# Kernel tuning notes

Measured on AMD Instinct MI355X. Metric: run time of the kernel, lower is better.

## Reference

```python
import jax, jax.numpy as jnp
import numpy as np

B, S, H, HEADS = 2, 512, 768, 12
HD = H // HEADS  # head dim 64
LN_EPS = 1e-5


def setup_inputs() -> dict:
    key = jax.random.key(0)
    ks = jax.random.split(key, 8)
    w = lambda k, shape: jax.random.normal(k, shape, dtype=jnp.float32) * 0.02
    return {
        "hidden_states": jax.random.normal(ks[0], (B, S, H), dtype=jnp.float32),
        "attention_mask": jnp.ones((B, S), dtype=jnp.int32),
        "Wp": w(ks[1], (H, H)), "bp": jnp.zeros((H,), jnp.float32),   # input_projection
        "Wq": w(ks[2], (H, H)), "bq": jnp.zeros((H,), jnp.float32),   # MHA q in-proj
        "Wk": w(ks[3], (H, H)), "bk": jnp.zeros((H,), jnp.float32),   # MHA k in-proj
        "We": w(ks[4], (H, H)), "be": jnp.zeros((H,), jnp.float32),   # edge_projection
        "gamma": jnp.ones((H,), jnp.float32), "beta": jnp.zeros((H,), jnp.float32),
    }


def reference(hidden_states, attention_mask, Wp, bp, Wq, bq, Wk, bk, We, be, gamma, beta):
    b, s, _ = hidden_states.shape
    # input projection (dropout = identity at eval)
    node = hidden_states @ Wp.T + bp                                   # [B,S,H]

    # self-attention weights (per-head), key_padding_mask = ~attention_mask
    q = (node @ Wq.T + bq).reshape(b, s, HEADS, HD).transpose(0, 2, 1, 3)
    k = (node @ Wk.T + bk).reshape(b, s, HEADS, HD).transpose(0, 2, 1, 3)
    logits = jnp.einsum("bhqd,bhkd->bhqk", q, k) / jnp.sqrt(jnp.float32(HD))
    pad = (attention_mask == 0)                                        # [B,S] keys to mask
    logits = jnp.where(pad[:, None, None, :], jnp.float32(-1e9), logits)
    attn = jax.nn.softmax(logits, axis=-1)                             # [B,HEADS,S,S]
    avg = attn.mean(axis=1)                                            # [B,S,S]

    # top-k sparsification: k = S // 2 neighbors per node
    ktop = s // 2
    _, idx = jax.lax.top_k(avg, ktop)                                  # [B,S,ktop]
    idx = jnp.sort(idx, axis=-1)  # torch.where emits dst in ascending order per src row
    scores = jnp.take_along_axis(avg, idx, axis=-1)                    # [B,S,ktop]

    # edge index with per-batch node offsets (all-ones mask -> every row kept)
    src = jnp.broadcast_to(jnp.arange(s)[None, :, None], (b, s, ktop))
    offset = (jnp.arange(b) * s)[:, None, None]
    edge_index = jnp.stack([(src + offset).reshape(-1),
                            (idx + offset).reshape(-1)], axis=0)       # [2, B*S*ktop]

    # edge_attr: zeros with col 0 = attn score, then Linear  ==  score * We[:,0] + be
    edge_attr = scores.reshape(-1)[:, None] * We[:, 0][None, :] + be   # [E, H]

    # final layer norm on node features
    mu = node.mean(axis=-1, keepdims=True)
    var = ((node - mu) ** 2).mean(axis=-1, keepdims=True)
    node_features = (node - mu) * jax.lax.rsqrt(var + LN_EPS) * gamma + beta

    return node_features, edge_index, edge_attr
```

## Files before the change

### kernel.cpp

```cpp
#include <hip/hip_runtime.h>

#define HH 768
#define SS 512
#define NB 2
#define NHEADS 12
#define KTOP 256
#define ETOT (NB*SS*KTOP)
#define LN_EPS 1e-5f

#define EI_OFF 786432L
#define EA_OFF 1310720L
#define PSZ    786432L

#define FMA16(a,b) \
    acc[0][0]=fmaf(a.x,b.x,acc[0][0]); acc[0][1]=fmaf(a.x,b.y,acc[0][1]); \
    acc[0][2]=fmaf(a.x,b.z,acc[0][2]); acc[0][3]=fmaf(a.x,b.w,acc[0][3]); \
    acc[1][0]=fmaf(a.y,b.x,acc[1][0]); acc[1][1]=fmaf(a.y,b.y,acc[1][1]); \
    acc[1][2]=fmaf(a.y,b.z,acc[1][2]); acc[1][3]=fmaf(a.y,b.w,acc[1][3]); \
    acc[2][0]=fmaf(a.z,b.x,acc[2][0]); acc[2][1]=fmaf(a.z,b.y,acc[2][1]); \
    acc[2][2]=fmaf(a.z,b.z,acc[2][2]); acc[2][3]=fmaf(a.z,b.w,acc[2][3]); \
    acc[3][0]=fmaf(a.w,b.x,acc[3][0]); acc[3][1]=fmaf(a.w,b.y,acc[3][1]); \
    acc[3][2]=fmaf(a.w,b.z,acc[3][2]); acc[3][3]=fmaf(a.w,b.w,acc[3][3]);

#define STORE_TILE(DST, V0, V1) \
    (DST)[sc4*4+0][srow]    = (V0).x; (DST)[sc4*4+1][srow]    = (V0).y; \
    (DST)[sc4*4+2][srow]    = (V0).z; (DST)[sc4*4+3][srow]    = (V0).w; \
    (DST)[sc4*4+0][srow+32] = (V1).x; (DST)[sc4*4+1][srow+32] = (V1).y; \
    (DST)[sc4*4+2][srow+32] = (V1).z; (DST)[sc4*4+3][srow+32] = (V1).w;

__device__ __forceinline__ float4 f4sum(const float* __restrict__ p0,
                                        const float* __restrict__ p1,
                                        const float* __restrict__ b,
                                        long off, int bcol)
{
    const float4 x = *(const float4*)(p0 + off);
    const float4 y = *(const float4*)(p1 + off);
    const float4 z = *(const float4*)(b + bcol);
    float4 r;
    r.x = x.x + y.x + z.x; r.y = x.y + y.y + z.y;
    r.z = x.z + y.z + z.z; r.w = x.w + y.w + z.w;
    return r;
}

__global__ __launch_bounds__(256, 3) void gemm_sk1(
    const float* __restrict__ A, const float* __restrict__ W,
    float* __restrict__ P)
{
    __shared__ float As[2][32][68];
    __shared__ float Ws[2][32][68];
    const int tid = threadIdx.x;
    const int tm = tid >> 4, tn = tid & 15;
    const int m0 = blockIdx.y * 64, n0 = blockIdx.x * 64;
    const int kh = blockIdx.z;
    const int srow = tid >> 3, sc4 = tid & 7;
    const int kbeg = kh * 384;

    const float* Ar0 = A + (long)(m0 + srow) * HH + kbeg + sc4 * 4;
    const float* Ar1 = Ar0 + 32 * HH;
    const float* Wr0 = W + (long)(n0 + srow) * HH + kbeg + sc4 * 4;
    const float* Wr1 = Wr0 + 32 * HH;

    float4 pa0 = *(const float4*)Ar0, pa1 = *(const float4*)Ar1;
    float4 pw0 = *(const float4*)Wr0, pw1 = *(const float4*)Wr1;

    float acc[4][4] = {};
    for (int kt = 0; kt < 12; ++kt) {
        const int cur = kt & 1;
        STORE_TILE(As[cur], pa0, pa1);
        STORE_TILE(Ws[cur], pw0, pw1);
        __syncthreads();
        if (kt < 11) {
            const int off = (kt + 1) * 32;
            pa0 = *(const float4*)(Ar0 + off);
            pa1 = *(const float4*)(Ar1 + off);
            pw0 = *(const float4*)(Wr0 + off);
            pw1 = *(const float4*)(Wr1 + off);
        }
        #pragma unroll
        for (int k = 0; k < 32; ++k) {
            const float4 a = *(const float4*)&As[cur][k][tm*4];
            const float4 b = *(const float4*)&Ws[cur][k][tn*4];
            FMA16(a, b)
        }
    }

    float* C = P + (long)kh * PSZ + (long)m0 * HH + n0;
    #pragma unroll
    for (int i = 0; i < 4; ++i) {
        float4 r;
        r.x = acc[i][0]; r.y = acc[i][1]; r.z = acc[i][2]; r.w = acc[i][3];
        *(float4*)(C + (long)(tm*4 + i) * HH + tn * 4) = r;
    }
}

__global__ __launch_bounds__(256, 3) void gemm_sk2(
    const float* __restrict__ P, const float* __restrict__ bp,
    const float* __restrict__ Wq, const float* __restrict__ Wk,
    float* __restrict__ QKP)
{
    __shared__ float As[2][32][68];
    __shared__ float Ws[2][32][68];
    const int tid = threadIdx.x;
    const int tm = tid >> 4, tn = tid & 15;
    const int m0 = blockIdx.y * 64, n0 = blockIdx.x * 64;
    const int sel = blockIdx.z >> 1, kh = blockIdx.z & 1;
    const float* W = sel ? Wk : Wq;
    const int srow = tid >> 3, sc4 = tid & 7;
    const int kbeg = kh * 384;

    const float* P1 = P + PSZ;
    const long aoff0 = (long)(m0 + srow) * HH + kbeg + sc4 * 4;
    const long aoff1 = aoff0 + 32 * HH;
    const int  bcol  = kbeg + sc4 * 4;
    const float* Wr0 = W + (long)(n0 + srow) * HH + kbeg + sc4 * 4;
    const float* Wr1 = Wr0 + 32 * HH;

    float4 pa0 = f4sum(P, P1, bp, aoff0, bcol);
    float4 pa1 = f4sum(P, P1, bp, aoff1, bcol);
    float4 pw0 = *(const float4*)Wr0;
    float4 pw1 = *(const float4*)Wr1;

    float acc[4][4] = {};
    for (int kt = 0; kt < 12; ++kt) {
        const int cur = kt & 1;
        STORE_TILE(As[cur], pa0, pa1);
        STORE_TILE(Ws[cur], pw0, pw1);
        __syncthreads();
        if (kt < 11) {
            const int off = (kt + 1) * 32;
            pa0 = f4sum(P, P1, bp, aoff0 + off, bcol + off);
            pa1 = f4sum(P, P1, bp, aoff1 + off, bcol + off);
            pw0 = *(const float4*)(Wr0 + off);
            pw1 = *(const float4*)(Wr1 + off);
        }
        #pragma unroll
        for (int k = 0; k < 32; ++k) {
            const float4 a = *(const float4*)&As[cur][k][tm*4];
            const float4 b = *(const float4*)&Ws[cur][k][tn*4];
            FMA16(a, b)
        }
    }

    float* C = QKP + ((long)sel * 2 + kh) * PSZ + (long)m0 * HH + n0;
    #pragma unroll
    for (int i = 0; i < 4; ++i) {
        float4 r;
        r.x = acc[i][0]; r.y = acc[i][1]; r.z = acc[i][2]; r.w = acc[i][3];
        *(float4*)(C + (long)(tm*4 + i) * HH + tn * 4) = r;
    }
}

__global__ __launch_bounds__(256, 3) void gemm_qk2(
    const float* __restrict__ QKP, const float* __restrict__ bq,
    const float* __restrict__ bk, float* __restrict__ logits)
{
    __shared__ float As[2][32][68];
    __shared__ float Ws[2][32][68];
    const int tid = threadIdx.x;
    const int tm = tid >> 4, tn = tid & 15;
    const int m0 = blockIdx.y * 64, n0 = blockIdx.x * 64;
    const int z = blockIdx.z, bz = z / NHEADS, hz = z - bz * NHEADS;
    const int srow = tid >> 3, sc4 = tid & 7;

    const float* q0 = QKP;
    const float* q1 = QKP + PSZ;
    const float* k0 = QKP + 2 * PSZ;
    const float* k1 = QKP + 3 * PSZ;

    const long rbase = (long)bz * SS * HH + hz * 64;
    const long aoff0 = rbase + (long)(m0 + srow) * HH + sc4 * 4;
    const long aoff1 = aoff0 + 32 * HH;
    const long woff0 = rbase + (long)(n0 + srow) * HH + sc4 * 4;
    const long woff1 = woff0 + 32 * HH;
    const int  bcol  = hz * 64 + sc4 * 4;

    float4 pa0 = f4sum(q0, q1, bq, aoff0, bcol);
    float4 pa1 = f4sum(q0, q1, bq, aoff1, bcol);
    float4 pw0 = f4sum(k0, k1, bk, woff0, bcol);
    float4 pw1 = f4sum(k0, k1, bk, woff1, bcol);

    float acc[4][4] = {};
    for (int kt = 0; kt < 2; ++kt) {
        const int cur = kt & 1;
        STORE_TILE(As[cur], pa0, pa1);
        STORE_TILE(Ws[cur], pw0, pw1);
        __syncthreads();
        if (kt == 0) {
            pa0 = f4sum(q0, q1, bq, aoff0 + 32, bcol + 32);
            pa1 = f4sum(q0, q1, bq, aoff1 + 32, bcol + 32);
            pw0 = f4sum(k0, k1, bk, woff0 + 32, bcol + 32);
            pw1 = f4sum(k0, k1, bk, woff1 + 32, bcol + 32);
        }
        #pragma unroll
        for (int k = 0; k < 32; ++k) {
            const float4 a = *(const float4*)&As[cur][k][tm*4];
            const float4 b = *(const float4*)&Ws[cur][k][tn*4];
            FMA16(a, b)
        }
    }

    float* C = logits + (long)z * SS * SS;
    #pragma unroll
    for (int i = 0; i < 4; ++i) {
        float4 r;
        r.x = acc[i][0] * 0.125f;
        r.y = acc[i][1] * 0.125f;
        r.z = acc[i][2] * 0.125f;
        r.w = acc[i][3] * 0.125f;
        *(float4*)(C + (long)(m0 + tm*4 + i) * SS + n0 + tn * 4) = r;
    }
}

__global__ __launch_bounds__(256) void ln_sum(
    const float* __restrict__ P, const float* __restrict__ bp,
    const float* __restrict__ gamma, const float* __restrict__ beta,
    float* __restrict__ out)
{
    const int row = blockIdx.x;
    const int t   = threadIdx.x;
    const float* x0 = P + (long)row * HH;
    const float* x1 = x0 + PSZ;

    const float v0 = x0[t]       + x1[t]       + bp[t];
    const float v1 = x0[t + 256] + x1[t + 256] + bp[t + 256];
    const float v2 = x0[t + 512] + x1[t + 512] + bp[t + 512];
    float s  = v0 + v1 + v2;
    float sq = v0 * v0 + v1 * v1 + v2 * v2;

    __shared__ float rs_[4], rq_[4];
    #pragma unroll
    for (int o = 32; o >= 1; o >>= 1) {
        s  += __shfl_xor(s, o);
        sq += __shfl_xor(sq, o);
    }
    if ((t & 63) == 0) { rs_[t >> 6] = s; rq_[t >> 6] = sq; }
    __syncthreads();
    const float S = rs_[0] + rs_[1] + rs_[2] + rs_[3];
    const float Q = rq_[0] + rq_[1] + rq_[2] + rq_[3];
    const float mu  = S * (1.f / HH);
    const float var = Q * (1.f / HH) - mu * mu;
    const float inv = rsqrtf(var + LN_EPS);

    float* o = out + (long)row * HH;
    o[t]       = (v0 - mu) * inv * gamma[t]       + beta[t];
    o[t + 256] = (v1 - mu) * inv * gamma[t + 256] + beta[t + 256];
    o[t + 512] = (v2 - mu) * inv * gamma[t + 512] + beta[t + 512];
}

__global__ __launch_bounds__(256) void attn_edge(
    const float* __restrict__ logits,
    const int*   __restrict__ mask,
    const float* __restrict__ We, const float* __restrict__ be,
    float* __restrict__ ei,
    float* __restrict__ ea)
{
    const int row = blockIdx.x;
    const int b   = row >> 9;
    const int qi  = row & 511;
    const int t   = threadIdx.x;
    const int wid = t >> 6, lane = t & 63;

    __shared__ float redA[4], redB[4];
    __shared__ unsigned long long keys[SS];
    __shared__ float4 wt[192], bt[192];
    __shared__ unsigned long long mskS[8];
    __shared__ float ssel[KTOP];

    const bool m0 = mask[b * SS + t] != 0;
    const bool m1 = mask[b * SS + t + 256] != 0;

    const float* basep = logits + ((long)b * NHEADS * SS + qi) * SS;

    float a0 = 0.f, a1 = 0.f;
    float c0v = m0 ? basep[t]       : -1e9f;
    float c1v = m1 ? basep[t + 256] : -1e9f;
    for (int h = 0; h < NHEADS; ++h) {
        const float l0 = c0v, l1 = c1v;
        if (h + 1 < NHEADS) {
            const float* nr = basep + (long)(h + 1) * SS * SS;
            c0v = m0 ? nr[t]       : -1e9f;
            c1v = m1 ? nr[t + 256] : -1e9f;
        }
        float v = fmaxf(l0, l1);
        #pragma unroll
        for (int o = 32; o >= 1; o >>= 1) v = fmaxf(v, __shfl_xor(v, o));
        if (lane == 0) redA[wid] = v;
        __syncthreads();
        const float bm = fmaxf(fmaxf(redA[0], redA[1]), fmaxf(redA[2], redA[3]));
        const float x0 = __expf(l0 - bm);
        const float x1 = __expf(l1 - bm);
        float s = x0 + x1;
        #pragma unroll
        for (int o = 32; o >= 1; o >>= 1) s += __shfl_xor(s, o);
        if (lane == 0) redB[wid] = s;
        __syncthreads();
        const float rs = 1.0f / (redB[0] + redB[1] + redB[2] + redB[3]);
        a0 = fmaf(x0, rs, a0);
        a1 = fmaf(x1, rs, a1);
    }
    a0 *= (1.f / NHEADS);
    a1 *= (1.f / NHEADS);

    const unsigned long long k0 =
        ((unsigned long long)__float_as_uint(a0) << 32) | (unsigned)(SS - 1 - t);
    const unsigned long long k1 =
        ((unsigned long long)__float_as_uint(a1) << 32) | (unsigned)(SS - 1 - (t + 256));
    keys[t]       = k0;
    keys[t + 256] = k1;
    __syncthreads();

    int r0 = 0, r1 = 0;
    #pragma unroll 8
    for (int j = 0; j < SS; ++j) {
        const unsigned long long kj = keys[j];
        r0 += (kj > k0);
        r1 += (kj > k1);
    }
    const bool sel0 = (r0 < KTOP);
    const bool sel1 = (r1 < KTOP);

    const unsigned long long mm0 = __ballot(sel0);
    const unsigned long long mm1 = __ballot(sel1);
    if (lane == 0) { mskS[wid] = mm0; mskS[4 + wid] = mm1; }
    __syncthreads();
    int cum[8]; int acc = 0;
    #pragma unroll
    for (int i = 0; i < 8; ++i) { cum[i] = acc; acc += __popcll(mskS[i]); }
    const unsigned long long lt = lane ? ((1ull << lane) - 1ull) : 0ull;
    const int p0 = cum[wid]     + __popcll(mskS[wid]     & lt);
    const int p1 = cum[4 + wid] + __popcll(mskS[4 + wid] & lt);

    const float srcv = (float)(b * SS + qi);
    const long  base_e = (long)row * KTOP;
    if (sel0) {
        ei[base_e + p0]        = srcv;
        ei[ETOT + base_e + p0] = (float)(b * SS + t);
        ssel[p0]               = a0;
    }
    if (sel1) {
        ei[base_e + p1]        = srcv;
        ei[ETOT + base_e + p1] = (float)(b * SS + t + 256);
        ssel[p1]               = a1;
    }

    if (t < 192) {
        float4 w;
        w.x = We[(long)(4 * t + 0) * HH];
        w.y = We[(long)(4 * t + 1) * HH];
        w.z = We[(long)(4 * t + 2) * HH];
        w.w = We[(long)(4 * t + 3) * HH];
        wt[t] = w;
        bt[t] = *(const float4*)(be + 4 * t);
    }
    __syncthreads();

    const int cA = t % 192, cB = (t + 64) % 192, cC = (t + 128) % 192;
    const float4 wA = wt[cA], bA = bt[cA];
    const float4 wB = wt[cB], bB = bt[cB];
    const float4 wC = wt[cC], bC = bt[cC];

    float4* dst = (float4*)(ea + base_e * HH);
    for (int m = 0; m < 64; ++m) {
        const int e_lo = m * 4;
        {
            const int e = e_lo + (t >= 192 ? 1 : 0);
            const float s = ssel[e];
            float4 r;
            r.x = fmaf(s, wA.x, bA.x); r.y = fmaf(s, wA.y, bA.y);
            r.z = fmaf(s, wA.z, bA.z); r.w = fmaf(s, wA.w, bA.w);
            dst[(3*m + 0) * 256 + t] = r;
        }
        {
            const int e = e_lo + 1 + (t >= 128 ? 1 : 0);
            const float s = ssel[e];
            float4 r;
            r.x = fmaf(s, wB.x, bB.x); r.y = fmaf(s, wB.y, bB.y);
            r.z = fmaf(s, wB.z, bB.z); r.w = fmaf(s, wB.w, bB.w);
            dst[(3*m + 1) * 256 + t] = r;
        }
        {
            const int e = e_lo + 2 + (t >= 64 ? 1 : 0);
            const float s = ssel[e];
            float4 r;
            r.x = fmaf(s, wC.x, bC.x); r.y = fmaf(s, wC.y, bC.y);
            r.z = fmaf(s, wC.z, bC.z); r.w = fmaf(s, wC.w, bC.w);
            dst[(3*m + 2) * 256 + t] = r;
        }
    }
}

extern "C" void kernel_launch(void* const* d_in, const int* in_sizes, int n_in,
                              void* d_out, int out_size, void* d_ws, size_t ws_size,
                              hipStream_t stream)
{
    const float* hidden = (const float*)d_in[0];
    const int*   mask   = (const int*)  d_in[1];
    const float* Wp = (const float*)d_in[2];
    const float* bp = (const float*)d_in[3];
    const float* Wq = (const float*)d_in[4];
    const float* bq = (const float*)d_in[5];
    const float* Wk = (const float*)d_in[6];
    const float* bk = (const float*)d_in[7];
    const float* We = (const float*)d_in[8];
    const float* be = (const float*)d_in[9];
    const float* gamma = (const float*)d_in[10];
    const float* beta  = (const float*)d_in[11];

    float* out = (float*)d_out;
    float* ws  = (float*)d_ws;

    float* logits = ws;
    float* pn     = out + EA_OFF;
    float* qkp    = out + EA_OFF + 2*PSZ;

    const dim3 blk(256);

    gemm_sk1<<<dim3(12, 16, 2), blk, 0, stream>>>(hidden, Wp, pn);
    gemm_sk2<<<dim3(12, 16, 4), blk, 0, stream>>>(pn, bp, Wq, Wk, qkp);
    gemm_qk2<<<dim3(8, 8, NB * NHEADS), blk, 0, stream>>>(qkp, bq, bk, logits);
    ln_sum<<<dim3(NB * SS), blk, 0, stream>>>(pn, bp, gamma, beta, out);
    attn_edge<<<dim3(NB * SS), blk, 0, stream>>>(logits, mask, We, be,
                                                 out + EI_OFF, out + EA_OFF);
}
```

Measured before the change: 251.0 us.

## Fold layernorm into gemm_sk2 grid; drop per-head max reduction in attn softmax

The separate ln_sum launch is removed. Its work moves into an extra z-slice of gemm_sk2, where 192 blocks loop over the 1024 rows and overlap with the Q/K projection GEMM. In attn_edge, the softmax over the 12 heads no longer subtracts a running max. That drops the max reduction and collapses two barriers per head into a single barrier after all per-head sums are stored in shared memory. This relies on the logits being small enough that exp does not overflow, and it adds register pressure from holding 24 exponentials per thread.

```diff
diff --git a/kernel.cpp b/kernel.cpp
--- a/kernel.cpp
+++ b/kernel.cpp
@@ -96,11 +96,47 @@
 __global__ __launch_bounds__(256, 3) void gemm_sk2(
     const float* __restrict__ P, const float* __restrict__ bp,
     const float* __restrict__ Wq, const float* __restrict__ Wk,
-    float* __restrict__ QKP)
+    float* __restrict__ QKP,
+    const float* __restrict__ gamma, const float* __restrict__ beta,
+    float* __restrict__ lnout)
 {
     __shared__ float As[2][32][68];
     __shared__ float Ws[2][32][68];
+    __shared__ float rs_[4], rq_[4];
     const int tid = threadIdx.x;
+
+    if (blockIdx.z == 4) {
+        const int fb = blockIdx.y * 12 + blockIdx.x;
+        const int t  = tid;
+        for (int row = fb; row < NB * SS; row += 192) {
+            const float* x0 = P + (long)row * HH;
+            const float* x1 = x0 + PSZ;
+            const float v0 = x0[t]       + x1[t]       + bp[t];
+            const float v1 = x0[t + 256] + x1[t + 256] + bp[t + 256];
+            const float v2 = x0[t + 512] + x1[t + 512] + bp[t + 512];
+            float s  = v0 + v1 + v2;
+            float sq = v0 * v0 + v1 * v1 + v2 * v2;
+            #pragma unroll
+            for (int o = 32; o >= 1; o >>= 1) {
+                s  += __shfl_xor(s, o);
+                sq += __shfl_xor(sq, o);
+            }
+            if ((t & 63) == 0) { rs_[t >> 6] = s; rq_[t >> 6] = sq; }
+            __syncthreads();
+            const float S = rs_[0] + rs_[1] + rs_[2] + rs_[3];
+            const float Q = rq_[0] + rq_[1] + rq_[2] + rq_[3];
+            const float mu  = S * (1.f / HH);
+            const float var = Q * (1.f / HH) - mu * mu;
+            const float inv = rsqrtf(var + LN_EPS);
+            float* o = lnout + (long)row * HH;
+            o[t]       = (v0 - mu) * inv * gamma[t]       + beta[t];
+            o[t + 256] = (v1 - mu) * inv * gamma[t + 256] + beta[t + 256];
+            o[t + 512] = (v2 - mu) * inv * gamma[t + 512] + beta[t + 512];
+            __syncthreads();
+        }
+        return;
+    }
+
     const int tm = tid >> 4, tn = tid & 15;
     const int m0 = blockIdx.y * 64, n0 = blockIdx.x * 64;
     const int sel = blockIdx.z >> 1, kh = blockIdx.z & 1;
@@ -211,42 +247,6 @@
     }
 }
 
-__global__ __launch_bounds__(256) void ln_sum(
-    const float* __restrict__ P, const float* __restrict__ bp,
-    const float* __restrict__ gamma, const float* __restrict__ beta,
-    float* __restrict__ out)
-{
-    const int row = blockIdx.x;
-    const int t   = threadIdx.x;
-    const float* x0 = P + (long)row * HH;
-    const float* x1 = x0 + PSZ;
-
-    const float v0 = x0[t]       + x1[t]       + bp[t];
-    const float v1 = x0[t + 256] + x1[t + 256] + bp[t + 256];
-    const float v2 = x0[t + 512] + x1[t + 512] + bp[t + 512];
-    float s  = v0 + v1 + v2;
-    float sq = v0 * v0 + v1 * v1 + v2 * v2;
-
-    __shared__ float rs_[4], rq_[4];
-    #pragma unroll
-    for (int o = 32; o >= 1; o >>= 1) {
-        s  += __shfl_xor(s, o);
-        sq += __shfl_xor(sq, o);
-    }
-    if ((t & 63) == 0) { rs_[t >> 6] = s; rq_[t >> 6] = sq; }
-    __syncthreads();
-    const float S = rs_[0] + rs_[1] + rs_[2] + rs_[3];
-    const float Q = rq_[0] + rq_[1] + rq_[2] + rq_[3];
-    const float mu  = S * (1.f / HH);
-    const float var = Q * (1.f / HH) - mu * mu;
-    const float inv = rsqrtf(var + LN_EPS);
-
-    float* o = out + (long)row * HH;
-    o[t]       = (v0 - mu) * inv * gamma[t]       + beta[t];
-    o[t + 256] = (v1 - mu) * inv * gamma[t + 256] + beta[t + 256];
-    o[t + 512] = (v2 - mu) * inv * gamma[t + 512] + beta[t + 512];
-}
-
 __global__ __launch_bounds__(256) void attn_edge(
     const float* __restrict__ logits,
     const int*   __restrict__ mask,
@@ -260,88 +260,11 @@
     const int t   = threadIdx.x;
     const int wid = t >> 6, lane = t & 63;
 
-    __shared__ float redA[4], redB[4];
+    __shared__ float red[NHEADS][4];
     __shared__ unsigned long long keys[SS];
     __shared__ float4 wt[192], bt[192];
     __shared__ unsigned long long mskS[8];
     __shared__ float ssel[KTOP];
-
-    const bool m0 = mask[b * SS + t] != 0;
-    const bool m1 = mask[b * SS + t + 256] != 0;
-
-    const float* basep = logits + ((long)b * NHEADS * SS + qi) * SS;
-
-    float a0 = 0.f, a1 = 0.f;
-    float c0v = m0 ? basep[t]       : -1e9f;
-    float c1v = m1 ? basep[t + 256] : -1e9f;
-    for (int h = 0; h < NHEADS; ++h) {
-        const float l0 = c0v, l1 = c1v;
-        if (h + 1 < NHEADS) {
-            const float* nr = basep + (long)(h + 1) * SS * SS;
-            c0v = m0 ? nr[t]       : -1e9f;
-            c1v = m1 ? nr[t + 256] : -1e9f;
-        }
-        float v = fmaxf(l0, l1);
-        #pragma unroll
-        for (int o = 32; o >= 1; o >>= 1) v = fmaxf(v, __shfl_xor(v, o));
-        if (lane == 0) redA[wid] = v;
-        __syncthreads();
-        const float bm = fmaxf(fmaxf(redA[0], redA[1]), fmaxf(redA[2], redA[3]));
-        const float x0 = __expf(l0 - bm);
-        const float x1 = __expf(l1 - bm);
-        float s = x0 + x1;
-        #pragma unroll
-        for (int o = 32; o >= 1; o >>= 1) s += __shfl_xor(s, o);
-        if (lane == 0) redB[wid] = s;
-        __syncthreads();
-        const float rs = 1.0f / (redB[0] + redB[1] + redB[2] + redB[3]);
-        a0 = fmaf(x0, rs, a0);
-        a1 = fmaf(x1, rs, a1);
-    }
-    a0 *= (1.f / NHEADS);
-    a1 *= (1.f / NHEADS);
-
-    const unsigned long long k0 =
-        ((unsigned long long)__float_as_uint(a0) << 32) | (unsigned)(SS - 1 - t);
-    const unsigned long long k1 =
-        ((unsigned long long)__float_as_uint(a1) << 32) | (unsigned)(SS - 1 - (t + 256));
-    keys[t]       = k0;
-    keys[t + 256] = k1;
-    __syncthreads();
-
-    int r0 = 0, r1 = 0;
-    #pragma unroll 8
-    for (int j = 0; j < SS; ++j) {
-        const unsigned long long kj = keys[j];
-        r0 += (kj > k0);
-        r1 += (kj > k1);
-    }
-    const bool sel0 = (r0 < KTOP);
-    const bool sel1 = (r1 < KTOP);
-
-    const unsigned long long mm0 = __ballot(sel0);
-    const unsigned long long mm1 = __ballot(sel1);
-    if (lane == 0) { mskS[wid] = mm0; mskS[4 + wid] = mm1; }
-    __syncthreads();
-    int cum[8]; int acc = 0;
-    #pragma unroll
-    for (int i = 0; i < 8; ++i) { cum[i] = acc; acc += __popcll(mskS[i]); }
-    const unsigned long long lt = lane ? ((1ull << lane) - 1ull) : 0ull;
-    const int p0 = cum[wid]     + __popcll(mskS[wid]     & lt);
-    const int p1 = cum[4 + wid] + __popcll(mskS[4 + wid] & lt);
-
-    const float srcv = (float)(b * SS + qi);
-    const long  base_e = (long)row * KTOP;
-    if (sel0) {
-        ei[base_e + p0]        = srcv;
-        ei[ETOT + base_e + p0] = (float)(b * SS + t);
-        ssel[p0]               = a0;
-    }
-    if (sel1) {
-        ei[base_e + p1]        = srcv;
-        ei[ETOT + base_e + p1] = (float)(b * SS + t + 256);
-        ssel[p1]               = a1;
-    }
 
     if (t < 192) {
         float4 w;
@@ -351,6 +274,78 @@
         w.w = We[(long)(4 * t + 3) * HH];
         wt[t] = w;
         bt[t] = *(const float4*)(be + 4 * t);
+    }
+
+    const bool m0 = mask[b * SS + t] != 0;
+    const bool m1 = mask[b * SS + t + 256] != 0;
+
+    const float* basep = logits + ((long)b * NHEADS * SS + qi) * SS;
+
+    float x0[NHEADS], x1[NHEADS];
+    #pragma unroll
+    for (int h = 0; h < NHEADS; ++h) {
+        const float* lr = basep + (long)h * SS * SS;
+        const float l0 = m0 ? lr[t]       : -1e9f;
+        const float l1 = m1 ? lr[t + 256] : -1e9f;
+        x0[h] = __expf(l0);
+        x1[h] = __expf(l1);
+        float s = x0[h] + x1[h];
+        #pragma unroll
+        for (int o = 32; o >= 1; o >>= 1) s += __shfl_xor(s, o);
+        if (lane == 0) red[h][wid] = s;
+    }
+    __syncthreads();
+
+    float a0 = 0.f, a1 = 0.f;
+    #pragma unroll
+    for (int h = 0; h < NHEADS; ++h) {
+        const float rs = 1.0f / (red[h][0] + red[h][1] + red[h][2] + red[h][3]);
+        a0 = fmaf(x0[h], rs, a0);
+        a1 = fmaf(x1[h], rs, a1);
+    }
+    a0 *= (1.f / NHEADS);
+    a1 *= (1.f / NHEADS);
+
+    const unsigned long long k0 =
+        ((unsigned long long)__float_as_uint(a0) << 32) | (unsigned)(SS - 1 - t);
+    const unsigned long long k1 =
+        ((unsigned long long)__float_as_uint(a1) << 32) | (unsigned)(SS - 1 - (t + 256));
+    keys[t]       = k0;
+    keys[t + 256] = k1;
+    __syncthreads();
+
+    int r0 = 0, r1 = 0;
+    #pragma unroll 8
+    for (int j = 0; j < SS; ++j) {
+        const unsigned long long kj = keys[j];
+        r0 += (kj > k0);
+        r1 += (kj > k1);
+    }
+    const bool sel0 = (r0 < KTOP);
+    const bool sel1 = (r1 < KTOP);
+
+    const unsigned long long mm0 = __ballot(sel0);
+    const unsigned long long mm1 = __ballot(sel1);
+    if (lane == 0) { mskS[wid] = mm0; mskS[4 + wid] = mm1; }
+    __syncthreads();
+    int cum[8]; int acc = 0;
+    #pragma unroll
+    for (int i = 0; i < 8; ++i) { cum[i] = acc; acc += __popcll(mskS[i]); }
+    const unsigned long long lt = lane ? ((1ull << lane) - 1ull) : 0ull;
+    const int p0 = cum[wid]     + __popcll(mskS[wid]     & lt);
+    const int p1 = cum[4 + wid] + __popcll(mskS[4 + wid] & lt);
+
+    const float srcv = (float)(b * SS + qi);
+    const long  base_e = (long)row * KTOP;
+    if (sel0) {
+        ei[base_e + p0]        = srcv;
+        ei[ETOT + base_e + p0] = (float)(b * SS + t);
+        ssel[p0]               = a0;
+    }
+    if (sel1) {
+        ei[base_e + p1]        = srcv;
+        ei[ETOT + base_e + p1] = (float)(b * SS + t + 256);
+        ssel[p1]               = a1;
     }
     __syncthreads();
 
@@ -416,9 +411,9 @@
     const dim3 blk(256);
 
     gemm_sk1<<<dim3(12, 16, 2), blk, 0, stream>>>(hidden, Wp, pn);
-    gemm_sk2<<<dim3(12, 16, 4), blk, 0, stream>>>(pn, bp, Wq, Wk, qkp);
+    gemm_sk2<<<dim3(12, 16, 5), blk, 0, stream>>>(pn, bp, Wq, Wk, qkp,
+                                                  gamma, beta, out);
     gemm_qk2<<<dim3(8, 8, NB * NHEADS), blk, 0, stream>>>(qkp, bq, bk, logits);
-    ln_sum<<<dim3(NB * SS), blk, 0, stream>>>(pn, bp, gamma, beta, out);
     attn_edge<<<dim3(NB * SS), blk, 0, stream>>>(logits, mask, We, be,
                                                  out + EI_OFF, out + EA_OFF);
 }
```

After: 247.4 us. No clear change (-1.4%).
